# Performance work log

Hardware: AMD Instinct MI355X
Metric: run time of the kernel (lower is better)

## Reference

```python
import jax, jax.numpy as jnp
import numpy as np

B, N, D, H = 8, 4096, 1024, 16
HD = D // H
EPS = 1e-5  # torch layer_norm default


def setup_inputs() -> dict:
    key = jax.random.key(0)
    ks = jax.random.split(key, 18)
    s = 1.0 / np.sqrt(D)

    def lin(k):
        return jax.random.normal(k, (D, D), jnp.float32) * s, jnp.zeros((D,), jnp.float32)

    Wg_w, Wg_b = lin(ks[0])
    Wr_w, Wr_b = lin(ks[1])
    Wk_w, Wk_b = lin(ks[2])
    Wv_w, Wv_b = lin(ks[3])
    Wo_w, Wo_b = lin(ks[4])
    mg = jax.random.uniform(ks[5], (D,), jnp.float32)
    mr = jax.random.uniform(ks[6], (D,), jnp.float32)
    mk = jax.random.uniform(ks[7], (D,), jnp.float32)
    mv = jax.random.uniform(ks[8], (D,), jnp.float32)
    w = jax.random.normal(ks[9], (H, HD), jnp.float32)
    u = jax.random.normal(ks[10], (H, HD), jnp.float32)
    x = jax.random.normal(ks[11], (B, N, D), jnp.float32)
    return {"x": x, "Wg_w": Wg_w, "Wg_b": Wg_b, "Wr_w": Wr_w, "Wr_b": Wr_b,
            "Wk_w": Wk_w, "Wk_b": Wk_b, "Wv_w": Wv_w, "Wv_b": Wv_b,
            "Wo_w": Wo_w, "Wo_b": Wo_b, "mg": mg, "mr": mr, "mk": mk, "mv": mv,
            "w": w, "u": u}


def reference(x, Wg_w, Wg_b, Wr_w, Wr_b, Wk_w, Wk_b, Wv_w, Wv_b, Wo_w, Wo_b,
              mg, mr, mk, mv, w, u):
    b, n, d = x.shape
    x_shift = jnp.roll(x, shift=1, axis=1)  # torch.roll wraps: row 0 <- row N-1

    def mix(m, W, bias):
        return (m * x + (1.0 - m) * x_shift) @ W.T + bias

    g = mix(mg, Wg_w, Wg_b).reshape(b, n, H, HD)
    r = mix(mr, Wr_w, Wr_b).reshape(b, n, H, HD)
    k = mix(mk, Wk_w, Wk_b).reshape(b, n, H, HD)
    v = mix(mv, Wv_w, Wv_b).reshape(b, n, H, HD)

    kv = k * v  # [B,N,H,HD]
    decay = jnp.exp(-jnp.exp(w))  # [H,HD]

    # sequential decay scan over time: acc_t = decay*acc_{t-1} + kv_t
    kv_t = jnp.swapaxes(kv, 0, 1)  # [N,B,H,HD]

    def step(acc, kvt):
        acc = decay * acc + kvt
        return acc, acc

    _, accs = jax.lax.scan(step, jnp.zeros((b, H, HD), x.dtype), kv_t)
    wkv = jnp.swapaxes(accs, 0, 1) + u * kv  # [B,N,H,HD]

    rw = r * wkv
    mean = jnp.mean(rw, axis=-1, keepdims=True)
    var = jnp.var(rw, axis=-1, keepdims=True)
    ln = (rw - mean) * jax.lax.rsqrt(var + EPS)

    out = (jax.nn.sigmoid(g) * ln).reshape(b, n, d)
    return out @ Wo_w.T + Wo_b
```

## Files before the change

kernel.cpp:

```cpp
#include <hip/hip_runtime.h>
#include <stdint.h>

#define NB 8
#define NSEQ 4096
#define DMODEL 1024
#define NH 16
#define HDIM 64
#define MROWS (NB*NSEQ)
#define NCHUNK 64
#define CHUNKL (NSEQ/NCHUNK)

typedef unsigned short u16;
typedef float f32x4 __attribute__((ext_vector_type(4)));
typedef short bf16x8 __attribute__((ext_vector_type(8)));

__device__ __forceinline__ u16 f2b(float f) {
  unsigned int u = __builtin_bit_cast(unsigned int, f);
  u = (u + 0x7FFFu + ((u >> 16) & 1u)) >> 16;
  return (u16)u;
}
__device__ __forceinline__ float b2f(u16 s) {
  unsigned int u = ((unsigned int)s) << 16;
  return __builtin_bit_cast(float, u);
}

__device__ __forceinline__ void gload16(const void* g, void* l) {
  __builtin_amdgcn_global_load_lds(
      (const __attribute__((address_space(1))) void*)g,
      (__attribute__((address_space(3))) void*)l, 16, 0, 0);
}

__global__ __launch_bounds__(256) void cvt5(
    const float* __restrict__ a0, const float* __restrict__ a1,
    const float* __restrict__ a2, const float* __restrict__ a3,
    const float* __restrict__ a4,
    u16* __restrict__ b0, u16* __restrict__ b1, u16* __restrict__ b2,
    u16* __restrict__ b3, u16* __restrict__ b4)
{
  const int mat = blockIdx.x >> 7;
  const int blk = blockIdx.x & 127;
  const float* s; u16* d;
  switch (mat) {
    case 0: s = a0; d = b0; break;
    case 1: s = a1; d = b1; break;
    case 2: s = a2; d = b2; break;
    case 3: s = a3; d = b3; break;
    default: s = a4; d = b4; break;
  }
#pragma unroll
  for (int it = 0; it < 8; ++it) {
    const int idx = blk*8192 + it*1024 + threadIdx.x*4;
    const float4 v = *(const float4*)(s + idx);
    ushort4 o; o.x = f2b(v.x); o.y = f2b(v.y); o.z = f2b(v.z); o.w = f2b(v.w);
    *(ushort4*)(d + idx) = o;
  }
}

__global__ __launch_bounds__(256) void mix4_kernel(
    const float* __restrict__ X,
    const float* __restrict__ mg, const float* __restrict__ mr,
    const float* __restrict__ mk, const float* __restrict__ mv,
    u16* __restrict__ Ag, u16* __restrict__ Ar, u16* __restrict__ Ak, u16* __restrict__ Av)
{
  const int i = blockIdx.x*256 + threadIdx.x;
  const int row = i >> 7;
  const int c8 = (i & 127) << 3;
  const int nidx = row & (NSEQ-1);
  const int rowm1 = (nidx == 0) ? row + (NSEQ-1) : row - 1;
  const size_t xo = (size_t)row*DMODEL + c8;
  const size_t so = (size_t)rowm1*DMODEL + c8;
  float xv[8], sv[8], mm[8];
  *(float4*)&xv[0] = *(const float4*)(X + xo);
  *(float4*)&xv[4] = *(const float4*)(X + xo + 4);
  *(float4*)&sv[0] = *(const float4*)(X + so);
  *(float4*)&sv[4] = *(const float4*)(X + so + 4);

#define DO_MIX(MP, AP) { \
    *(float4*)&mm[0] = *(const float4*)(MP + c8); \
    *(float4*)&mm[4] = *(const float4*)(MP + c8 + 4); \
    bf16x8 o; \
    _Pragma("unroll") \
    for (int j = 0; j < 8; ++j) o[j] = (short)f2b(mm[j]*xv[j] + (1.f-mm[j])*sv[j]); \
    *(bf16x8*)(AP + xo) = o; }

  DO_MIX(mg, Ag)
  DO_MIX(mr, Ar)
  DO_MIX(mk, Ak)
  DO_MIX(mv, Av)
#undef DO_MIX
}

#define FENCE asm volatile("" ::: "memory")
#define BAR() { FENCE; __builtin_amdgcn_s_barrier(); FENCE; }
#define PRIO1 __builtin_amdgcn_s_setprio(1)
#define PRIO0 __builtin_amdgcn_s_setprio(0)
#define VM6 asm volatile("s_waitcnt vmcnt(6)" ::: "memory")
#define VM4 asm volatile("s_waitcnt vmcnt(4)" ::: "memory")
#define VM0 asm volatile("s_waitcnt vmcnt(0)" ::: "memory")

template<int OUTBF>
__global__ __launch_bounds__(512, 2) void gemm256(
    const u16* __restrict__ Abf, const u16* __restrict__ Wb,
    const float* __restrict__ bias, float* __restrict__ outF, u16* __restrict__ outB)
{
  __shared__ __align__(16) char lds[131072];
  const int tid = threadIdx.x;
  const int wave = tid >> 6, lane = tid & 63;
  const int wm = wave >> 2, wn = wave & 3;
  const int rla = lane & 15, kgrp = lane >> 4;

  const int wg = blockIdx.x;
  const int xcd = wg & 7, slot = wg >> 3;
  const int by = xcd*16 + (slot >> 2);
  const int bx = slot & 3;

  const int F0 = (wave*2+0)*1024 + lane*16;
  const int F1 = (wave*2+1)*1024 + lane*16;
  const int r0 = F0 >> 6, r1 = F1 >> 6;
  const int c80 = ((F0 >> 4) & 3) ^ ((r0 >> 1) & 3);
  const int c81 = ((F1 >> 4) & 3) ^ ((r1 >> 1) & 3);
  const char* Ab = (const char*)Abf;
  const char* Bbp = (const char*)Wb;
  const unsigned ga0 = (unsigned)by*256*2048 + r0*2048 + c80*16;
  const unsigned ga1 = (unsigned)by*256*2048 + r1*2048 + c81*16;
  const unsigned gb0 = (unsigned)bx*256*2048 + r0*2048 + c80*16;
  const unsigned gb1 = (unsigned)bx*256*2048 + r1*2048 + c81*16;
  const int dst0 = wave*2048;
  const int dst1 = wave*2048 + 1024;

  f32x4 acc[8][4];
#pragma unroll
  for (int i = 0; i < 8; ++i)
#pragma unroll
    for (int j = 0; j < 4; ++j) acc[i][j] = f32x4{0.f,0.f,0.f,0.f};
  bf16x8 af[8], bfr[4];
  const int lane_ds = rla*64 + ((kgrp ^ ((rla>>1)&3)) << 4);

#define LDS_A(D,KK) (lds + (D)*32768 + (KK)*16384)
#define LDS_B(D,KK) (lds + 65536 + (D)*32768 + (KK)*16384)
#define LDA(D,KK) { _Pragma("unroll") for (int mi_ = 0; mi_ < 8; ++mi_) \
    af[mi_] = *(const bf16x8*)(LDS_A(D,KK) + (wm*128 + mi_*16)*64 + lane_ds); }
#define LDB(P,D,KK) { _Pragma("unroll") for (int j_ = 0; j_ < 2; ++j_) \
    bfr[(P)*2+j_] = *(const bf16x8*)(LDS_B(D,KK) + (wn*64 + ((P)*2+j_)*16)*64 + lane_ds); }
#define MM(P) { _Pragma("unroll") for (int mi_ = 0; mi_ < 8; ++mi_) { \
    acc[mi_][(P)*2+0] = __builtin_amdgcn_mfma_f32_16x16x32_bf16(af[mi_], bfr[(P)*2+0], acc[mi_][(P)*2+0], 0,0,0); \
    acc[mi_][(P)*2+1] = __builtin_amdgcn_mfma_f32_16x16x32_bf16(af[mi_], bfr[(P)*2+1], acc[mi_][(P)*2+1], 0,0,0); } }
#define STAGE(ISB, T, KK) { \
    const char* g_ = (ISB) ? Bbp : Ab; \
    const unsigned o0_ = ((ISB) ? gb0 : ga0) + (T)*128 + (KK)*64; \
    const unsigned o1_ = ((ISB) ? gb1 : ga1) + (T)*128 + (KK)*64; \
    char* l_ = (ISB) ? LDS_B((T)&1, KK) : LDS_A((T)&1, KK); \
    gload16(g_ + o0_, l_ + dst0); \
    gload16(g_ + o1_, l_ + dst1); }

  STAGE(0, 0, 0); STAGE(1, 0, 0); STAGE(0, 0, 1); STAGE(1, 0, 1);
  VM4;
  STAGE(0, 1, 0); STAGE(1, 1, 0); STAGE(0, 1, 1);
  VM6;
  BAR();

  for (int i = 0; i < 8; ++i) {
    const int t1 = 2*i+1, t2 = 2*i+2, t3 = 2*i+3;
    const bool s2 = (i < 7);
    LDA(0,0); LDB(0,0,0); STAGE(1, t1, 1);
    BAR(); PRIO1; MM(0); PRIO0; BAR();
    LDB(1,0,0); if (s2) STAGE(0, t2, 0);
    BAR(); PRIO1; MM(1); PRIO0; BAR();
    LDA(0,1); LDB(0,0,1); if (s2) STAGE(1, t2, 0);
    BAR(); PRIO1; MM(0); PRIO0; BAR();
    LDB(1,0,1); if (s2) STAGE(0, t2, 1);
    BAR(); PRIO1; MM(1); PRIO0;
    if (i == 7) { VM0; } else { VM6; }
    BAR();
    LDA(1,0); LDB(0,1,0); if (s2) STAGE(1, t2, 1);
    BAR(); PRIO1; MM(0); PRIO0; BAR();
    LDB(1,1,0); if (s2) STAGE(0, t3, 0);
    BAR(); PRIO1; MM(1); PRIO0; BAR();
    LDA(1,1); LDB(0,1,1); if (s2) STAGE(1, t3, 0);
    BAR(); PRIO1; MM(0); PRIO0; BAR();
    LDB(1,1,1); if (s2) STAGE(0, t3, 1);
    BAR(); PRIO1; MM(1); PRIO0; VM6; BAR();
  }

  float bval[4];
#pragma unroll
  for (int ni = 0; ni < 4; ++ni) bval[ni] = bias[bx*256 + wn*64 + ni*16 + rla];
#pragma unroll
  for (int mi = 0; mi < 8; ++mi) {
#pragma unroll
    for (int ni = 0; ni < 4; ++ni) {
      const int gr0 = by*256 + wm*128 + mi*16 + kgrp*4;
      const int gc  = bx*256 + wn*64 + ni*16 + rla;
#pragma unroll
      for (int q = 0; q < 4; ++q) {
        const float v = acc[mi][ni][q] + bval[ni];
        const size_t o = (size_t)(gr0 + q)*DMODEL + gc;
        if (OUTBF) outB[o] = f2b(v);
        else       outF[o] = v;
      }
    }
  }
#undef LDS_A
#undef LDS_B
#undef LDA
#undef LDB
#undef MM
#undef STAGE
}

__global__ __launch_bounds__(256) void scan_pass1(
    const u16* __restrict__ kbuf, const u16* __restrict__ vbuf,
    const float* __restrict__ w, float* __restrict__ chunkAcc)
{
  const int c = blockIdx.x & (NCHUNK-1);
  const int b = blockIdx.x >> 6;
  const int hh = threadIdx.x >> 4;
  const int ch0 = (threadIdx.x & 15) << 2;
  const int hch = hh*HDIM + ch0;

  float dd[4];
#pragma unroll
  for (int j = 0; j < 4; ++j) dd[j] = expf(-expf(w[hch + j]));

  const size_t base = ((size_t)b*NSEQ + (size_t)c*CHUNKL)*DMODEL + hch;
  float acc[4] = {0.f, 0.f, 0.f, 0.f};
#pragma unroll 2
  for (int i = 0; i < CHUNKL; ++i) {
    const size_t idx = base + (size_t)i*DMODEL;
    const ushort4 k4 = *(const ushort4*)(kbuf + idx);
    const ushort4 v4 = *(const ushort4*)(vbuf + idx);
    acc[0] = dd[0]*acc[0] + b2f(k4.x)*b2f(v4.x);
    acc[1] = dd[1]*acc[1] + b2f(k4.y)*b2f(v4.y);
    acc[2] = dd[2]*acc[2] + b2f(k4.z)*b2f(v4.z);
    acc[3] = dd[3]*acc[3] + b2f(k4.w)*b2f(v4.w);
  }
  float4 o; o.x = acc[0]; o.y = acc[1]; o.z = acc[2]; o.w = acc[3];
  *(float4*)&chunkAcc[((size_t)(b*NH + hh)*NCHUNK + c)*HDIM + ch0] = o;
}

__global__ __launch_bounds__(64) void scan_pass2(
    const float* __restrict__ chunkAcc, float* __restrict__ carryPrev,
    const float* __restrict__ w)
{
  const int bh = blockIdx.x;
  const int h = bh & (NH-1);
  const int lanehd = threadIdx.x;
  const float e = expf(w[h*HDIM + lanehd]);
  const float dL = expf(-e * (float)CHUNKL);
  const size_t base = (size_t)bh*NCHUNK*HDIM + lanehd;
  float carry = 0.f;
  for (int c = 0; c < NCHUNK; ++c) {
    carryPrev[base + (size_t)c*HDIM] = carry;
    carry = chunkAcc[base + (size_t)c*HDIM] + dL*carry;
  }
}

__global__ __launch_bounds__(256) void scan_pass3(
    const u16* __restrict__ kbuf, const u16* __restrict__ vbuf,
    const u16* __restrict__ rbuf, const u16* __restrict__ gbuf,
    u16* __restrict__ hbuf, const float* __restrict__ carryPrev,
    const float* __restrict__ w, const float* __restrict__ u)
{
  const int c = blockIdx.x & (NCHUNK-1);
  const int b = blockIdx.x >> 6;
  const int hh = threadIdx.x >> 4;
  const int ch0 = (threadIdx.x & 15) << 2;
  const int hch = hh*HDIM + ch0;

  float dd[4], uv[4], carry[4], fac[4], acc[4];
#pragma unroll
  for (int j = 0; j < 4; ++j) {
    dd[j] = expf(-expf(w[hch + j]));
    uv[j] = u[hch + j];
    fac[j] = dd[j];
    acc[j] = 0.f;
  }
  const float4 cv = *(const float4*)&carryPrev[((size_t)(b*NH + hh)*NCHUNK + c)*HDIM + ch0];
  carry[0] = cv.x; carry[1] = cv.y; carry[2] = cv.z; carry[3] = cv.w;

  const size_t base = ((size_t)b*NSEQ + (size_t)c*CHUNKL)*DMODEL + hch;
#pragma unroll 2
  for (int i = 0; i < CHUNKL; ++i) {
    const size_t idx = base + (size_t)i*DMODEL;
    const ushort4 k4 = *(const ushort4*)(kbuf + idx);
    const ushort4 v4 = *(const ushort4*)(vbuf + idx);
    const ushort4 r4 = *(const ushort4*)(rbuf + idx);
    const ushort4 g4 = *(const ushort4*)(gbuf + idx);
    float rw[4];
    float s1 = 0.f, s2 = 0.f;
    {
      const float kv = b2f(k4.x)*b2f(v4.x);
      acc[0] = dd[0]*acc[0] + kv;
      const float wkv = acc[0] + fac[0]*carry[0] + uv[0]*kv;
      fac[0] *= dd[0];
      rw[0] = b2f(r4.x)*wkv; s1 += rw[0]; s2 += rw[0]*rw[0];
    }
    {
      const float kv = b2f(k4.y)*b2f(v4.y);
      acc[1] = dd[1]*acc[1] + kv;
      const float wkv = acc[1] + fac[1]*carry[1] + uv[1]*kv;
      fac[1] *= dd[1];
      rw[1] = b2f(r4.y)*wkv; s1 += rw[1]; s2 += rw[1]*rw[1];
    }
    {
      const float kv = b2f(k4.z)*b2f(v4.z);
      acc[2] = dd[2]*acc[2] + kv;
      const float wkv = acc[2] + fac[2]*carry[2] + uv[2]*kv;
      fac[2] *= dd[2];
      rw[2] = b2f(r4.z)*wkv; s1 += rw[2]; s2 += rw[2]*rw[2];
    }
    {
      const float kv = b2f(k4.w)*b2f(v4.w);
      acc[3] = dd[3]*acc[3] + kv;
      const float wkv = acc[3] + fac[3]*carry[3] + uv[3]*kv;
      fac[3] *= dd[3];
      rw[3] = b2f(r4.w)*wkv; s1 += rw[3]; s2 += rw[3]*rw[3];
    }
#pragma unroll
    for (int off = 8; off >= 1; off >>= 1) {
      s1 += __shfl_xor(s1, off);
      s2 += __shfl_xor(s2, off);
    }
    const float mean = s1 * (1.f/64.f);
    const float var = s2 * (1.f/64.f) - mean*mean;
    const float rstd = rsqrtf(var + 1e-5f);
    ushort4 o;
    o.x = f2b((rw[0]-mean)*rstd * (1.f/(1.f+expf(-b2f(g4.x)))));
    o.y = f2b((rw[1]-mean)*rstd * (1.f/(1.f+expf(-b2f(g4.y)))));
    o.z = f2b((rw[2]-mean)*rstd * (1.f/(1.f+expf(-b2f(g4.z)))));
    o.w = f2b((rw[3]-mean)*rstd * (1.f/(1.f+expf(-b2f(g4.w)))));
    *(ushort4*)(hbuf + idx) = o;
  }
}

extern "C" void kernel_launch(void* const* d_in, const int* in_sizes, int n_in,
                              void* d_out, int out_size, void* d_ws, size_t ws_size,
                              hipStream_t stream)
{
  const float* x   = (const float*)d_in[0];
  const float* WgW = (const float*)d_in[1];
  const float* Wgb = (const float*)d_in[2];
  const float* WrW = (const float*)d_in[3];
  const float* Wrb = (const float*)d_in[4];
  const float* WkW = (const float*)d_in[5];
  const float* Wkb = (const float*)d_in[6];
  const float* WvW = (const float*)d_in[7];
  const float* Wvb = (const float*)d_in[8];
  const float* WoW = (const float*)d_in[9];
  const float* Wob = (const float*)d_in[10];
  const float* mg  = (const float*)d_in[11];
  const float* mr  = (const float*)d_in[12];
  const float* mk  = (const float*)d_in[13];
  const float* mv  = (const float*)d_in[14];
  const float* w   = (const float*)d_in[15];
  const float* u   = (const float*)d_in[16];
  char* ws = (char*)d_ws;

  const size_t WBB = (size_t)DMODEL*DMODEL*2;
  u16* WgB = (u16*)(ws + 0*WBB);
  u16* WrB = (u16*)(ws + 1*WBB);
  u16* WkB = (u16*)(ws + 2*WBB);
  u16* WvB = (u16*)(ws + 3*WBB);
  u16* WoB = (u16*)(ws + 4*WBB);
  size_t off = 5*WBB;
  const size_t EL = (size_t)MROWS*DMODEL;

  char* amBase = ws + off;
  u16* Amg = (u16*)(amBase);
  u16* Amr = (u16*)(amBase + EL*2);
  u16* Amk = (u16*)(amBase + EL*4);
  u16* Amv = (u16*)(amBase + EL*6);
  u16* kbuf = Amg;
  u16* vbuf = Amr;
  u16* hbuf = Amk;
  off += EL*8;
  u16* gbuf = (u16*)(ws + off);   off += EL*2;
  u16* rbuf = (u16*)(ws + off);   off += EL*2;
  float* chunkAcc  = (float*)(ws + off); off += (size_t)NB*NH*NCHUNK*HDIM*4;
  float* carryPrev = (float*)(ws + off); off += (size_t)NB*NH*NCHUNK*HDIM*4;

  cvt5<<<640, 256, 0, stream>>>(WgW, WrW, WkW, WvW, WoW, WgB, WrB, WkB, WvB, WoB);

  mix4_kernel<<<(int)(EL/8/256), 256, 0, stream>>>(x, mg, mr, mk, mv, Amg, Amr, Amk, Amv);

  gemm256<1><<<512, 512, 0, stream>>>(Amg, WgB, Wgb, nullptr, gbuf);
  gemm256<1><<<512, 512, 0, stream>>>(Amr, WrB, Wrb, nullptr, rbuf);
  gemm256<1><<<512, 512, 0, stream>>>(Amk, WkB, Wkb, nullptr, kbuf);
  gemm256<1><<<512, 512, 0, stream>>>(Amv, WvB, Wvb, nullptr, vbuf);

  scan_pass1<<<NB*NCHUNK, 256, 0, stream>>>(kbuf, vbuf, w, chunkAcc);
  scan_pass2<<<NB*NH, 64, 0, stream>>>(chunkAcc, carryPrev, w);
  scan_pass3<<<NB*NCHUNK, 256, 0, stream>>>(kbuf, vbuf, rbuf, gbuf, hbuf, carryPrev, w, u);

  gemm256<0><<<512, 512, 0, stream>>>(hbuf, WoB, Wob, (float*)d_out, nullptr);
}
```

Measured before the change: 580.8 us.

## Fuse three-pass chunked scan into one kernel with flag-based chunk carry propagation

Replaces the three scan kernels with a single kernel. Each block computes its chunk's local aggregate, publishes it with a release flag, then spin-waits on all earlier chunks' flags and folds their aggregates with powers of the chunk decay to get its carry. This removes a serial 64-step pass and one kernel launch, and lets the second sweep over k/v hit cache. The mix kernel also now handles 16 columns per thread instead of 8. The cost is a quadratic lookback, and spin-waiting can deadlock if later blocks become resident before earlier ones; that is unlikely with 512 blocks, which should all be resident at once.

```diff
diff --git a/kernel.cpp b/kernel.cpp
--- a/kernel.cpp
+++ b/kernel.cpp
@@ -63,25 +63,29 @@
     u16* __restrict__ Ag, u16* __restrict__ Ar, u16* __restrict__ Ak, u16* __restrict__ Av)
 {
   const int i = blockIdx.x*256 + threadIdx.x;
-  const int row = i >> 7;
-  const int c8 = (i & 127) << 3;
+  const int row = i >> 6;
+  const int c16 = (i & 63) << 4;
   const int nidx = row & (NSEQ-1);
   const int rowm1 = (nidx == 0) ? row + (NSEQ-1) : row - 1;
-  const size_t xo = (size_t)row*DMODEL + c8;
-  const size_t so = (size_t)rowm1*DMODEL + c8;
-  float xv[8], sv[8], mm[8];
-  *(float4*)&xv[0] = *(const float4*)(X + xo);
-  *(float4*)&xv[4] = *(const float4*)(X + xo + 4);
-  *(float4*)&sv[0] = *(const float4*)(X + so);
-  *(float4*)&sv[4] = *(const float4*)(X + so + 4);
+  const size_t xo = (size_t)row*DMODEL + c16;
+  const size_t so = (size_t)rowm1*DMODEL + c16;
+  float xv[16], sv[16], mm[16];
+#pragma unroll
+  for (int q = 0; q < 4; ++q) {
+    *(float4*)&xv[q*4] = *(const float4*)(X + xo + q*4);
+    *(float4*)&sv[q*4] = *(const float4*)(X + so + q*4);
+  }
 
 #define DO_MIX(MP, AP) { \
-    *(float4*)&mm[0] = *(const float4*)(MP + c8); \
-    *(float4*)&mm[4] = *(const float4*)(MP + c8 + 4); \
-    bf16x8 o; \
     _Pragma("unroll") \
-    for (int j = 0; j < 8; ++j) o[j] = (short)f2b(mm[j]*xv[j] + (1.f-mm[j])*sv[j]); \
-    *(bf16x8*)(AP + xo) = o; }
+    for (int q = 0; q < 4; ++q) *(float4*)&mm[q*4] = *(const float4*)(MP + c16 + q*4); \
+    bf16x8 o0, o1; \
+    _Pragma("unroll") \
+    for (int j = 0; j < 8; ++j) o0[j] = (short)f2b(mm[j]*xv[j] + (1.f-mm[j])*sv[j]); \
+    _Pragma("unroll") \
+    for (int j = 0; j < 8; ++j) o1[j] = (short)f2b(mm[8+j]*xv[8+j] + (1.f-mm[8+j])*sv[8+j]); \
+    *(bf16x8*)(AP + xo) = o0; \
+    *(bf16x8*)(AP + xo + 8) = o1; }
 
   DO_MIX(mg, Ag)
   DO_MIX(mr, Ar)
@@ -208,9 +212,13 @@
 #undef STAGE
 }
 
-__global__ __launch_bounds__(256) void scan_pass1(
+__global__ void zero_flags(int* flags) { flags[threadIdx.x] = 0; }
+
+__global__ __launch_bounds__(256) void scan_fused(
     const u16* __restrict__ kbuf, const u16* __restrict__ vbuf,
-    const float* __restrict__ w, float* __restrict__ chunkAcc)
+    const u16* __restrict__ rbuf, const u16* __restrict__ gbuf,
+    u16* __restrict__ hbuf, const float* __restrict__ w,
+    const float* __restrict__ u, float* __restrict__ agg, int* __restrict__ flags)
 {
   const int c = blockIdx.x & (NCHUNK-1);
   const int b = blockIdx.x >> 6;
@@ -218,11 +226,17 @@
   const int ch0 = (threadIdx.x & 15) << 2;
   const int hch = hh*HDIM + ch0;
 
-  float dd[4];
-#pragma unroll
-  for (int j = 0; j < 4; ++j) dd[j] = expf(-expf(w[hch + j]));
+  float dd[4], dL[4], uv[4];
+#pragma unroll
+  for (int j = 0; j < 4; ++j) {
+    const float e = expf(w[hch + j]);
+    dd[j] = expf(-e);
+    dL[j] = expf(-e * (float)CHUNKL);
+    uv[j] = u[hch + j];
+  }
 
   const size_t base = ((size_t)b*NSEQ + (size_t)c*CHUNKL)*DMODEL + hch;
+
   float acc[4] = {0.f, 0.f, 0.f, 0.f};
 #pragma unroll 2
   for (int i = 0; i < CHUNKL; ++i) {
@@ -234,51 +248,28 @@
     acc[2] = dd[2]*acc[2] + b2f(k4.z)*b2f(v4.z);
     acc[3] = dd[3]*acc[3] + b2f(k4.w)*b2f(v4.w);
   }
-  float4 o; o.x = acc[0]; o.y = acc[1]; o.z = acc[2]; o.w = acc[3];
-  *(float4*)&chunkAcc[((size_t)(b*NH + hh)*NCHUNK + c)*HDIM + ch0] = o;
-}
-
-__global__ __launch_bounds__(64) void scan_pass2(
-    const float* __restrict__ chunkAcc, float* __restrict__ carryPrev,
-    const float* __restrict__ w)
-{
-  const int bh = blockIdx.x;
-  const int h = bh & (NH-1);
-  const int lanehd = threadIdx.x;
-  const float e = expf(w[h*HDIM + lanehd]);
-  const float dL = expf(-e * (float)CHUNKL);
-  const size_t base = (size_t)bh*NCHUNK*HDIM + lanehd;
-  float carry = 0.f;
-  for (int c = 0; c < NCHUNK; ++c) {
-    carryPrev[base + (size_t)c*HDIM] = carry;
-    carry = chunkAcc[base + (size_t)c*HDIM] + dL*carry;
-  }
-}
-
-__global__ __launch_bounds__(256) void scan_pass3(
-    const u16* __restrict__ kbuf, const u16* __restrict__ vbuf,
-    const u16* __restrict__ rbuf, const u16* __restrict__ gbuf,
-    u16* __restrict__ hbuf, const float* __restrict__ carryPrev,
-    const float* __restrict__ w, const float* __restrict__ u)
-{
-  const int c = blockIdx.x & (NCHUNK-1);
-  const int b = blockIdx.x >> 6;
-  const int hh = threadIdx.x >> 4;
-  const int ch0 = (threadIdx.x & 15) << 2;
-  const int hch = hh*HDIM + ch0;
-
-  float dd[4], uv[4], carry[4], fac[4], acc[4];
-#pragma unroll
-  for (int j = 0; j < 4; ++j) {
-    dd[j] = expf(-expf(w[hch + j]));
-    uv[j] = u[hch + j];
-    fac[j] = dd[j];
-    acc[j] = 0.f;
-  }
-  const float4 cv = *(const float4*)&carryPrev[((size_t)(b*NH + hh)*NCHUNK + c)*HDIM + ch0];
-  carry[0] = cv.x; carry[1] = cv.y; carry[2] = cv.z; carry[3] = cv.w;
-
-  const size_t base = ((size_t)b*NSEQ + (size_t)c*CHUNKL)*DMODEL + hch;
+  {
+    float4 o; o.x = acc[0]; o.y = acc[1]; o.z = acc[2]; o.w = acc[3];
+    *(float4*)(agg + (size_t)blockIdx.x*DMODEL + hch) = o;
+  }
+  __threadfence();
+  __syncthreads();
+  if (threadIdx.x == 0)
+    __hip_atomic_store(&flags[blockIdx.x], 1, __ATOMIC_RELEASE, __HIP_MEMORY_SCOPE_AGENT);
+
+  float carry[4] = {0.f, 0.f, 0.f, 0.f};
+  float wf[4] = {1.f, 1.f, 1.f, 1.f};
+  const int b0 = b*NCHUNK;
+  for (int j = c-1; j >= 0; --j) {
+    while (__hip_atomic_load(&flags[b0 + j], __ATOMIC_ACQUIRE, __HIP_MEMORY_SCOPE_AGENT) == 0)
+      __builtin_amdgcn_s_sleep(2);
+    const float4 a4 = *(const float4*)(agg + (size_t)(b0 + j)*DMODEL + hch);
+    carry[0] += wf[0]*a4.x; carry[1] += wf[1]*a4.y;
+    carry[2] += wf[2]*a4.z; carry[3] += wf[3]*a4.w;
+    wf[0] *= dL[0]; wf[1] *= dL[1]; wf[2] *= dL[2]; wf[3] *= dL[3];
+  }
+
+  float acc2[4] = {carry[0], carry[1], carry[2], carry[3]};
 #pragma unroll 2
   for (int i = 0; i < CHUNKL; ++i) {
     const size_t idx = base + (size_t)i*DMODEL;
@@ -290,31 +281,23 @@
     float s1 = 0.f, s2 = 0.f;
     {
       const float kv = b2f(k4.x)*b2f(v4.x);
-      acc[0] = dd[0]*acc[0] + kv;
-      const float wkv = acc[0] + fac[0]*carry[0] + uv[0]*kv;
-      fac[0] *= dd[0];
-      rw[0] = b2f(r4.x)*wkv; s1 += rw[0]; s2 += rw[0]*rw[0];
+      acc2[0] = dd[0]*acc2[0] + kv;
+      rw[0] = b2f(r4.x)*(acc2[0] + uv[0]*kv); s1 += rw[0]; s2 += rw[0]*rw[0];
     }
     {
       const float kv = b2f(k4.y)*b2f(v4.y);
-      acc[1] = dd[1]*acc[1] + kv;
-      const float wkv = acc[1] + fac[1]*carry[1] + uv[1]*kv;
-      fac[1] *= dd[1];
-      rw[1] = b2f(r4.y)*wkv; s1 += rw[1]; s2 += rw[1]*rw[1];
+      acc2[1] = dd[1]*acc2[1] + kv;
+      rw[1] = b2f(r4.y)*(acc2[1] + uv[1]*kv); s1 += rw[1]; s2 += rw[1]*rw[1];
     }
     {
       const float kv = b2f(k4.z)*b2f(v4.z);
-      acc[2] = dd[2]*acc[2] + kv;
-      const float wkv = acc[2] + fac[2]*carry[2] + uv[2]*kv;
-      fac[2] *= dd[2];
-      rw[2] = b2f(r4.z)*wkv; s1 += rw[2]; s2 += rw[2]*rw[2];
+      acc2[2] = dd[2]*acc2[2] + kv;
+      rw[2] = b2f(r4.z)*(acc2[2] + uv[2]*kv); s1 += rw[2]; s2 += rw[2]*rw[2];
     }
     {
       const float kv = b2f(k4.w)*b2f(v4.w);
-      acc[3] = dd[3]*acc[3] + kv;
-      const float wkv = acc[3] + fac[3]*carry[3] + uv[3]*kv;
-      fac[3] *= dd[3];
-      rw[3] = b2f(r4.w)*wkv; s1 += rw[3]; s2 += rw[3]*rw[3];
+      acc2[3] = dd[3]*acc2[3] + kv;
+      rw[3] = b2f(r4.w)*(acc2[3] + uv[3]*kv); s1 += rw[3]; s2 += rw[3]*rw[3];
     }
 #pragma unroll
     for (int off = 8; off >= 1; off >>= 1) {
@@ -376,21 +359,20 @@
   off += EL*8;
   u16* gbuf = (u16*)(ws + off);   off += EL*2;
   u16* rbuf = (u16*)(ws + off);   off += EL*2;
-  float* chunkAcc  = (float*)(ws + off); off += (size_t)NB*NH*NCHUNK*HDIM*4;
-  float* carryPrev = (float*)(ws + off); off += (size_t)NB*NH*NCHUNK*HDIM*4;
+  float* agg = (float*)(ws + off); off += (size_t)NB*NCHUNK*DMODEL*4;
+  int* flags = (int*)(ws + off);   off += (size_t)NB*NCHUNK*4;
 
   cvt5<<<640, 256, 0, stream>>>(WgW, WrW, WkW, WvW, WoW, WgB, WrB, WkB, WvB, WoB);
 
-  mix4_kernel<<<(int)(EL/8/256), 256, 0, stream>>>(x, mg, mr, mk, mv, Amg, Amr, Amk, Amv);
+  mix4_kernel<<<(int)(EL/16/256), 256, 0, stream>>>(x, mg, mr, mk, mv, Amg, Amr, Amk, Amv);
 
   gemm256<1><<<512, 512, 0, stream>>>(Amg, WgB, Wgb, nullptr, gbuf);
   gemm256<1><<<512, 512, 0, stream>>>(Amr, WrB, Wrb, nullptr, rbuf);
   gemm256<1><<<512, 512, 0, stream>>>(Amk, WkB, Wkb, nullptr, kbuf);
   gemm256<1><<<512, 512, 0, stream>>>(Amv, WvB, Wvb, nullptr, vbuf);
 
-  scan_pass1<<<NB*NCHUNK, 256, 0, stream>>>(kbuf, vbuf, w, chunkAcc);
-  scan_pass2<<<NB*NH, 64, 0, stream>>>(chunkAcc, carryPrev, w);
-  scan_pass3<<<NB*NCHUNK, 256, 0, stream>>>(kbuf, vbuf, rbuf, gbuf, hbuf, carryPrev, w, u);
+  zero_flags<<<1, NB*NCHUNK, 0, stream>>>(flags);
+  scan_fused<<<NB*NCHUNK, 256, 0, stream>>>(kbuf, vbuf, rbuf, gbuf, hbuf, w, u, agg, flags);
 
   gemm256<0><<<512, 512, 0, stream>>>(hbuf, WoB, Wob, (float*)d_out, nullptr);
 }
```

New measurement: 1.137 ms. 95.7% more time.
